# Performance work log

Measured on AMD Instinct MI355X. Metric: run time of the kernel, lower is better.

## Reference

```python
import jax, jax.numpy as jnp
import numpy as np

N = 20000   # nodes
E = 160000  # edges
D = 128     # out_dim == in_dim
H = 8       # heads
DK = D // H # 16


def setup_inputs() -> dict:
    key = jax.random.key(0)
    ks = jax.random.split(key, 16)
    f = lambda i, shape, s=1.0: jax.random.normal(ks[i], shape, dtype=jnp.float32) * s
    z = lambda shape: jnp.zeros(shape, dtype=jnp.float32)
    return {
        "x_txt": f(0, (N, D)), "x_img": f(1, (N, D)), "x_s": f(2, (N, D)),
        "Wk": f(3, (D, D), 0.05), "bk": z((D,)),
        "Wq": f(4, (D, D), 0.05), "bq": z((D,)),
        "Wv": f(5, (D, D), 0.05), "bv": z((D,)),
        "Wa": f(6, (D, D), 0.05), "ba": z((D,)),
        "rel_att": f(7, (H, DK, DK), 0.25),
        "rel_msg": f(8, (H, DK, DK), 0.25),
        "rel_pri": jnp.ones((H,), jnp.float32),
        "wm_txt": f(9, (H, DK, DK), 0.25),
        "wm_img": f(10, (H, DK, DK), 0.25),
        "wm_s": f(11, (H, DK, DK), 0.25),
        "skip": jnp.ones((1,), jnp.float32),
        "src": jax.random.randint(ks[12], (E,), 0, N),
        "dst": jax.random.randint(ks[13], (E,), 0, N),
    }


def reference(x_txt, x_img, x_s, Wk, bk, Wq, bq, Wv, bv, Wa, ba,
              rel_att, rel_msg, rel_pri, wm_txt, wm_img, wm_s, skip, src, dst):
    n_heads, dk = rel_att.shape[0], rel_att.shape[1]
    n_nodes = x_txt.shape[0]
    sqrt_dk = jnp.sqrt(jnp.asarray(dk, jnp.float32))

    def proj(x, W, b):
        return (x @ W + b).reshape(n_nodes, n_heads, dk)

    xs = (x_txt, x_img, x_s)
    k = [proj(x, Wk, bk)[src] for x in xs]  # [E,H,dk] gathered at src
    q = [proj(x, Wq, bq)[dst] for x in xs]  # [E,H,dk] gathered at dst
    v = [proj(x, Wv, bv)[src] for x in xs]

    # cross-modal lambda: per-edge modality alignment softmax (over the 3 modalities)
    wm = (wm_txt, wm_img, wm_s)
    lam_scores = jnp.stack(
        [jnp.einsum('ehd,hdf,ehf->eh', k[m], wm[m], q[m]) for m in range(3)], axis=0)
    lam = jax.nn.softmax(lam_scores, axis=0)  # [3,E,H]

    # edge attention logits (scaled *10 as in reduce_func) and relation-msg values
    att = [jnp.einsum('ehd,hdf,ehf->eh', k[m], rel_att, q[m]) * rel_pri / sqrt_dk * 10.0
           for m in range(3)]
    vmsg = [jnp.einsum('ehd,hdf->ehf', v[m], rel_msg) for m in range(3)]

    align = -(jnp.abs(att[0] - att[1]) + jnp.abs(att[0] - att[2])
              + jnp.abs(att[1] - att[2])) / 3.0

    def seg_softmax(x):  # softmax over edges sharing the same dst node
        m = jax.ops.segment_max(x, dst, num_segments=n_nodes)
        m = jnp.where(jnp.isfinite(m), m, 0.0)
        e = jnp.exp(x - m[dst])
        s = jax.ops.segment_sum(e, dst, num_segments=n_nodes)
        s = jnp.where(s == 0.0, 1.0, s)
        return e / s[dst]

    beta2 = seg_softmax(align)
    sm = [seg_softmax(a) for a in att]
    beta1 = sm[0] * lam[0] + sm[1] * lam[1] + sm[2] * lam[2]
    beta = seg_softmax(beta1 * beta2)  # [E,H]

    alpha = jax.nn.sigmoid(skip)  # [1]
    outs = []
    for m in range(3):
        h = jax.ops.segment_sum(beta[..., None] * vmsg[m], dst,
                                num_segments=n_nodes).reshape(n_nodes, -1)
        outs.append((h @ Wa + ba) * alpha + xs[m] * (1.0 - alpha))
    return tuple(outs)
```

## Files before the change

kernel.cpp:

```cpp
#include <hip/hip_runtime.h>

#define D 128
#define NH 8

typedef __bf16 bf16x8 __attribute__((ext_vector_type(8)));
typedef unsigned short ushortx8 __attribute__((ext_vector_type(8)));
typedef float floatx4 __attribute__((ext_vector_type(4)));

__device__ __forceinline__ float bf2f(unsigned short u) {
  union { unsigned int i; float f; } x; x.i = ((unsigned int)u) << 16; return x.f;
}
__device__ __forceinline__ unsigned short f2bf(float f) {
  union { float f; unsigned int i; } x; x.f = f;
  unsigned int i = x.i;
  return (unsigned short)((i + 0x7FFFu + ((i >> 16) & 1u)) >> 16);
}
__device__ __forceinline__ void acc2(unsigned int ku, unsigned int qu, float& s) {
  union { unsigned int i; float f; } a, b;
  a.i = ku << 16;          b.i = qu << 16;          s += a.f * b.f;
  a.i = ku & 0xffff0000u;  b.i = qu & 0xffff0000u;  s += a.f * b.f;
}

__global__ __launch_bounds__(256) void k_misc(
    const float* __restrict__ Wk, const float* __restrict__ bk,
    const float* __restrict__ Wq, const float* __restrict__ bq,
    const float* __restrict__ Wv, const float* __restrict__ bv,
    const float* __restrict__ rel_att, const float* __restrict__ rel_msg,
    const float* __restrict__ rel_pri,
    const float* __restrict__ wm0, const float* __restrict__ wm1,
    const float* __restrict__ wm2,
    unsigned short* __restrict__ Wt_all, float* __restrict__ bias_all,
    const int* __restrict__ dst, int* __restrict__ counts, int E)
{
  int b = blockIdx.x;
  if (b >= 384) {
    int e = (b - 384) * 256 + threadIdx.x;
    if (e < E) atomicAdd(&counts[dst[e]], 1);
    return;
  }
  int gid = b * 256 + threadIdx.x;
  if (gid >= 6 * 128 * 128) return;
  int p = gid >> 14;
  int idx = gid & 16383;
  int c = idx >> 7, k = idx & 127;
  int h = c >> 4, r = c & 15;
  float wsum = 0.f, bsum = 0.f;
  if (p == 0) {
    wsum = Wk[k * 128 + c];
    bsum = bk[c];
  } else if (p <= 4) {
    const float* M = (p == 1) ? rel_att : ((p == 2) ? wm0 : ((p == 3) ? wm1 : wm2));
#pragma unroll
    for (int f = 0; f < 16; f++) {
      float mv = M[h * 256 + r * 16 + f];
      wsum += Wq[k * 128 + h * 16 + f] * mv;
      bsum += bq[h * 16 + f] * mv;
    }
    if (p == 1) { float sc = rel_pri[h] * 2.5f; wsum *= sc; bsum *= sc; }
  } else {
#pragma unroll
    for (int d = 0; d < 16; d++) {
      float mv = rel_msg[h * 256 + d * 16 + r];
      wsum += Wv[k * 128 + h * 16 + d] * mv;
      bsum += bv[h * 16 + d] * mv;
    }
  }
  Wt_all[(size_t)p * 16384 + c * 128 + k] = f2bf(wsum);
  if (k == 0) bias_all[p * 128 + c] = bsum;
}

__global__ __launch_bounds__(256) void k_proj(
    const float* __restrict__ x0, const float* __restrict__ x1,
    const float* __restrict__ x2,
    const unsigned short* __restrict__ Wt_all, const float* __restrict__ bias_all,
    unsigned short* __restrict__ P, int N)
{
  __shared__ __attribute__((aligned(16))) unsigned short Wt[128 * 136];
  int m = blockIdx.y;
  const float* X = (m == 0) ? x0 : ((m == 1) ? x1 : x2);
  int tid = threadIdx.x;
  int wave = tid >> 6, lane = tid & 63;
  int quad = lane >> 4, l16 = lane & 15;
  int row0 = blockIdx.x * 64 + wave * 16;
  int arow = row0 + l16; if (arow >= N) arow = N - 1;
  const float* ap = X + (size_t)arow * D;
  bf16x8 afr[4];
#pragma unroll
  for (int kk4 = 0; kk4 < 4; kk4++) {
    float4 f0 = *(const float4*)(ap + kk4 * 32 + quad * 8);
    float4 f1 = *(const float4*)(ap + kk4 * 32 + quad * 8 + 4);
    ushortx8 uu;
    uu[0]=f2bf(f0.x); uu[1]=f2bf(f0.y); uu[2]=f2bf(f0.z); uu[3]=f2bf(f0.w);
    uu[4]=f2bf(f1.x); uu[5]=f2bf(f1.y); uu[6]=f2bf(f1.z); uu[7]=f2bf(f1.w);
    afr[kk4] = __builtin_bit_cast(bf16x8, uu);
  }
  for (int pt = 0; pt < 4; pt++) {
    int wp = (pt == 0) ? 0 : ((pt == 1) ? 1 : ((pt == 2) ? (2 + m) : 5));
    const unsigned short* Wsrc = Wt_all + (size_t)wp * 16384;
    const float* B = bias_all + wp * 128;
    __syncthreads();
#pragma unroll
    for (int it = 0; it < 8; it++) {
      int idx = it * 256 + tid;
      int c = idx >> 4, kc = (idx & 15) << 3;
      *(uint4*)(&Wt[c * 136 + kc]) = *(const uint4*)(&Wsrc[c * 128 + kc]);
    }
    __syncthreads();
    floatx4 acc[8];
#pragma unroll
    for (int ct = 0; ct < 8; ct++) acc[ct] = (floatx4)0.f;
#pragma unroll
    for (int kk4 = 0; kk4 < 4; kk4++) {
#pragma unroll
      for (int ct = 0; ct < 8; ct++) {
        uint4 bu = *(const uint4*)(&Wt[(ct * 16 + l16) * 136 + kk4 * 32 + quad * 8]);
        bf16x8 bf = __builtin_bit_cast(bf16x8, bu);
        acc[ct] = __builtin_amdgcn_mfma_f32_16x16x32_bf16(afr[kk4], bf, acc[ct], 0, 0, 0);
      }
    }
    unsigned short* Pout = P + (size_t)(pt * 3 + m) * N * D;
#pragma unroll
    for (int ct = 0; ct < 8; ct++) {
      int col = ct * 16 + l16;
      float bias = B[col];
#pragma unroll
      for (int i = 0; i < 4; i++) {
        int r = row0 + quad * 4 + i;
        if (r < N) Pout[(size_t)r * D + col] = f2bf(acc[ct][i] + bias);
      }
    }
  }
}

__global__ __launch_bounds__(1024) void k_scan_part(
    const int* __restrict__ counts, int* __restrict__ row_start,
    int* __restrict__ partials, int N)
{
  __shared__ int wsum[16];
  int tid = threadIdx.x;
  int gi = blockIdx.x * 1024 + tid;
  int v = (gi < N) ? counts[gi] : 0;
  int lane = tid & 63, wid = tid >> 6;
  int x = v;
#pragma unroll
  for (int off = 1; off < 64; off <<= 1) {
    int y = __shfl_up(x, off, 64);
    if (lane >= off) x += y;
  }
  if (lane == 63) wsum[wid] = x;
  __syncthreads();
  if (wid == 0) {
    int ws = (lane < 16) ? wsum[lane] : 0;
#pragma unroll
    for (int off = 1; off < 16; off <<= 1) {
      int y = __shfl_up(ws, off, 64);
      if (lane >= off) ws += y;
    }
    if (lane < 16) wsum[lane] = ws;
  }
  __syncthreads();
  int excl = x - v + (wid > 0 ? wsum[wid - 1] : 0);
  if (gi <= N) row_start[gi] = excl;
  if (tid == 0) partials[blockIdx.x] = wsum[15];
}

__global__ __launch_bounds__(1024) void k_scan_fix(
    int* __restrict__ row_start, const int* __restrict__ partials, int N, int nb)
{
  __shared__ int offs[64];
  int tid = threadIdx.x;
  if (tid == 0) {
    int acc = 0;
    for (int b = 0; b < nb; b++) { offs[b] = acc; acc += partials[b]; }
  }
  __syncthreads();
  for (int i = tid; i <= N; i += 1024) row_start[i] += offs[i >> 10];
}

__global__ void k_scatter(const int* __restrict__ dst, const int* __restrict__ src,
                          const int* __restrict__ row_start,
                          int* __restrict__ cursor, int* __restrict__ src_sorted, int E) {
  int e = blockIdx.x * 256 + threadIdx.x;
  if (e < E) {
    int d = dst[e];
    int pos = atomicAdd(&cursor[d], 1);
    src_sorted[row_start[d] + pos] = src[e];
  }
}

__device__ __forceinline__ void edge_vals(
    const unsigned short* __restrict__ P, size_t Nsz, int s, int h,
    const uint4 (&qa)[3][2], const uint4 (&qw)[3][2],
    float (&av)[3], float (&lv)[3])
{
#pragma unroll
  for (int m = 0; m < 3; m++) {
    const unsigned short* kp = P + ((size_t)m * Nsz + s) * 128 + h * 16;
    uint4 k0 = *(const uint4*)kp, k1 = *(const uint4*)(kp + 8);
    const unsigned int* ka = (const unsigned int*)&k0;
    const unsigned int* kb = (const unsigned int*)&k1;
    const unsigned int* a0 = (const unsigned int*)&qa[m][0];
    const unsigned int* a1 = (const unsigned int*)&qa[m][1];
    const unsigned int* w0 = (const unsigned int*)&qw[m][0];
    const unsigned int* w1 = (const unsigned int*)&qw[m][1];
    float da = 0.f, dw = 0.f;
#pragma unroll
    for (int j = 0; j < 4; j++) {
      acc2(ka[j], a0[j], da); acc2(kb[j], a1[j], da);
      acc2(ka[j], w0[j], dw); acc2(kb[j], w1[j], dw);
    }
    av[m] = da;
    lv[m] = dw;
  }
  float mx = fmaxf(lv[0], fmaxf(lv[1], lv[2]));
  float e0 = __expf(lv[0] - mx), e1 = __expf(lv[1] - mx), e2 = __expf(lv[2] - mx);
  float inv = 1.f / (e0 + e1 + e2);
  lv[0] = e0 * inv; lv[1] = e1 * inv; lv[2] = e2 * inv;
}

__global__ __launch_bounds__(256) void k_node(
    const unsigned short* __restrict__ P,
    const int* __restrict__ row_start, const int* __restrict__ srcs,
    unsigned short* __restrict__ hagg, int N, int E)
{
  int tid = threadIdx.x;
  int wave = tid >> 6, lane = tid & 63;
  int n = blockIdx.x * 4 + wave;
  if (n >= N) return;
  int ro = row_start[n];
  int deg = row_start[n + 1] - ro;
  float acc00 = 0, acc01 = 0, acc10 = 0, acc11 = 0, acc20 = 0, acc21 = 0;
  if (deg > 0) {
    int h = lane & 7, slot = lane >> 3;
    size_t Nsz = (size_t)N;
    uint4 qa[3][2], qw[3][2];
#pragma unroll
    for (int m = 0; m < 3; m++) {
      const unsigned short* qap = P + ((size_t)(3 + m) * Nsz + n) * 128 + h * 16;
      const unsigned short* qwp = P + ((size_t)(6 + m) * Nsz + n) * 128 + h * 16;
      qa[m][0] = *(const uint4*)qap; qa[m][1] = *(const uint4*)(qap + 8);
      qw[m][0] = *(const uint4*)qwp; qw[m][1] = *(const uint4*)(qwp + 8);
    }
    int nch = (deg + 7) >> 3;
    float cX0[4] = {}, cX1[4] = {}, cX2[4] = {}, cEa[4] = {}, cT[4] = {};
    int cS[4] = {};
    float sA0 = 0, sA1 = 0, sA2 = 0, sAl = 0;
#pragma unroll
    for (int c = 0; c < 4; c++) {
      int idx = c * 8 + slot;
      if (c < nch && idx < deg) {
        int s = srcs[ro + idx]; cS[c] = s;
        float av[3], lv[3];
        edge_vals(P, Nsz, s, h, qa, qw, av, lv);
        float e0 = __expf(av[0]), e1 = __expf(av[1]), e2 = __expf(av[2]);
        float align = -(fabsf(av[0]-av[1]) + fabsf(av[0]-av[2]) + fabsf(av[1]-av[2])) * (1.f/3.f);
        float ea = __expf(align);
        cX0[c] = lv[0] * e0; cX1[c] = lv[1] * e1; cX2[c] = lv[2] * e2; cEa[c] = ea;
        sA0 += e0; sA1 += e1; sA2 += e2; sAl += ea;
      }
    }
    for (int c = 4; c < nch; c++) {
      int idx = c * 8 + slot;
      if (idx < deg) {
        int s = srcs[ro + idx];
        float av[3], lv[3];
        edge_vals(P, Nsz, s, h, qa, qw, av, lv);
        float align = -(fabsf(av[0]-av[1]) + fabsf(av[0]-av[2]) + fabsf(av[1]-av[2])) * (1.f/3.f);
        sA0 += __expf(av[0]); sA1 += __expf(av[1]); sA2 += __expf(av[2]);
        sAl += __expf(align);
      }
    }
#pragma unroll
    for (int off = 8; off < 64; off <<= 1) {
      sA0 += __shfl_xor(sA0, off, 64);
      sA1 += __shfl_xor(sA1, off, 64);
      sA2 += __shfl_xor(sA2, off, 64);
      sAl += __shfl_xor(sAl, off, 64);
    }
    float rA0 = 1.f / fmaxf(sA0, 1e-30f), rA1 = 1.f / fmaxf(sA1, 1e-30f);
    float rA2 = 1.f / fmaxf(sA2, 1e-30f), rAl = 1.f / fmaxf(sAl, 1e-30f);
    float sT = 0;
#pragma unroll
    for (int c = 0; c < 4; c++) {
      int idx = c * 8 + slot;
      if (c < nch && idx < deg) {
        float t = (cX0[c] * rA0 + cX1[c] * rA1 + cX2[c] * rA2) * (cEa[c] * rAl);
        cT[c] = t;
        sT += __expf(t);
      }
    }
    for (int c = 4; c < nch; c++) {
      int idx = c * 8 + slot;
      if (idx < deg) {
        int s = srcs[ro + idx];
        float av[3], lv[3];
        edge_vals(P, Nsz, s, h, qa, qw, av, lv);
        float align = -(fabsf(av[0]-av[1]) + fabsf(av[0]-av[2]) + fabsf(av[1]-av[2])) * (1.f/3.f);
        float t = (lv[0]*__expf(av[0])*rA0 + lv[1]*__expf(av[1])*rA1 + lv[2]*__expf(av[2])*rA2)
                  * (__expf(align) * rAl);
        sT += __expf(t);
      }
    }
#pragma unroll
    for (int off = 8; off < 64; off <<= 1) sT += __shfl_xor(sT, off, 64);
    float rT = 1.f / fmaxf(sT, 1e-30f);
    const unsigned int* Pu = (const unsigned int*)P;
    int hl = lane >> 3;
#pragma unroll
    for (int c = 0; c < 4; c++) {
      if (c < nch) {
        int idx = c * 8 + slot;
        float beta = (idx < deg) ? __expf(cT[c]) * rT : 0.f;
        int sv = cS[c];
        float bj[8]; int sj[8];
#pragma unroll
        for (int jj = 0; jj < 8; jj++) {
          bj[jj] = __shfl(beta, jj * 8 + hl, 64);
          sj[jj] = __shfl(sv, jj * 8, 64);
        }
#pragma unroll
        for (int jj = 0; jj < 8; jj++) {
          size_t base9 = ((size_t)9 * Nsz + sj[jj]) * 64 + lane;
          unsigned int u0 = Pu[base9];
          unsigned int u1 = Pu[base9 + Nsz * 64];
          unsigned int u2 = Pu[base9 + 2 * Nsz * 64];
          float b = bj[jj];
          acc00 += b * bf2f((unsigned short)u0); acc01 += b * bf2f((unsigned short)(u0 >> 16));
          acc10 += b * bf2f((unsigned short)u1); acc11 += b * bf2f((unsigned short)(u1 >> 16));
          acc20 += b * bf2f((unsigned short)u2); acc21 += b * bf2f((unsigned short)(u2 >> 16));
        }
      }
    }
    for (int c = 4; c < nch; c++) {
      int idx = c * 8 + slot;
      float beta = 0.f; int sv = 0;
      if (idx < deg) {
        sv = srcs[ro + idx];
        float av[3], lv[3];
        edge_vals(P, Nsz, sv, h, qa, qw, av, lv);
        float align = -(fabsf(av[0]-av[1]) + fabsf(av[0]-av[2]) + fabsf(av[1]-av[2])) * (1.f/3.f);
        float t = (lv[0]*__expf(av[0])*rA0 + lv[1]*__expf(av[1])*rA1 + lv[2]*__expf(av[2])*rA2)
                  * (__expf(align) * rAl);
        beta = __expf(t) * rT;
      }
      int jmax = min(8, deg - c * 8);
      for (int jj = 0; jj < jmax; jj++) {
        float b = __shfl(beta, jj * 8 + hl, 64);
        int s = __shfl(sv, jj * 8, 64);
        size_t base9 = ((size_t)9 * Nsz + s) * 64 + lane;
        unsigned int u0 = Pu[base9];
        unsigned int u1 = Pu[base9 + Nsz * 64];
        unsigned int u2 = Pu[base9 + 2 * Nsz * 64];
        acc00 += b * bf2f((unsigned short)u0); acc01 += b * bf2f((unsigned short)(u0 >> 16));
        acc10 += b * bf2f((unsigned short)u1); acc11 += b * bf2f((unsigned short)(u1 >> 16));
        acc20 += b * bf2f((unsigned short)u2); acc21 += b * bf2f((unsigned short)(u2 >> 16));
      }
    }
  }
  unsigned int* ho = (unsigned int*)hagg;
  ho[((size_t)0 * N + n) * 64 + lane] = ((unsigned int)f2bf(acc01) << 16) | f2bf(acc00);
  ho[((size_t)1 * N + n) * 64 + lane] = ((unsigned int)f2bf(acc11) << 16) | f2bf(acc10);
  ho[((size_t)2 * N + n) * 64 + lane] = ((unsigned int)f2bf(acc21) << 16) | f2bf(acc20);
}

__global__ __launch_bounds__(256) void k_out(
    const unsigned short* __restrict__ Hagg, const float* __restrict__ Wa,
    const float* __restrict__ ba,
    const float* __restrict__ x0, const float* __restrict__ x1,
    const float* __restrict__ x2, const float* __restrict__ skip,
    float* __restrict__ out, int N)
{
  __shared__ __attribute__((aligned(16))) unsigned short Wt[128 * 136];
  int m = blockIdx.y;
  const float* X = (m == 0) ? x0 : ((m == 1) ? x1 : x2);
  int tid = threadIdx.x;
#pragma unroll
  for (int it = 0; it < 16; it++) {
    int idx = it * 256 + tid;
    int k = idx >> 5, c4 = (idx & 31) << 2;
    float4 w = *(const float4*)(&Wa[k * 128 + c4]);
    Wt[(c4 + 0) * 136 + k] = f2bf(w.x);
    Wt[(c4 + 1) * 136 + k] = f2bf(w.y);
    Wt[(c4 + 2) * 136 + k] = f2bf(w.z);
    Wt[(c4 + 3) * 136 + k] = f2bf(w.w);
  }
  __syncthreads();
  float alpha = 1.f / (1.f + __expf(-skip[0]));
  float oma = 1.f - alpha;
  int wave = tid >> 6, lane = tid & 63;
  int quad = lane >> 4, l16 = lane & 15;
  int row0 = blockIdx.x * 64 + wave * 16;
  int arow = row0 + l16; if (arow >= N) arow = N - 1;
  const unsigned short* hp = Hagg + ((size_t)m * N + arow) * D;
  floatx4 acc[8];
#pragma unroll
  for (int ct = 0; ct < 8; ct++) acc[ct] = (floatx4)0.f;
#pragma unroll
  for (int kk = 0; kk < 128; kk += 32) {
    uint4 au = *(const uint4*)(hp + kk + quad * 8);
    bf16x8 af = __builtin_bit_cast(bf16x8, au);
#pragma unroll
    for (int ct = 0; ct < 8; ct++) {
      uint4 bu = *(const uint4*)(&Wt[(ct * 16 + l16) * 136 + kk + quad * 8]);
      bf16x8 bf = __builtin_bit_cast(bf16x8, bu);
      acc[ct] = __builtin_amdgcn_mfma_f32_16x16x32_bf16(af, bf, acc[ct], 0, 0, 0);
    }
  }
  float* om = out + (size_t)m * N * D;
#pragma unroll
  for (int ct = 0; ct < 8; ct++) {
    int col = ct * 16 + l16;
    float bias = ba[col];
#pragma unroll
    for (int i = 0; i < 4; i++) {
      int r = row0 + quad * 4 + i;
      if (r < N) {
        om[(size_t)r * D + col] =
            (acc[ct][i] + bias) * alpha + X[(size_t)r * D + col] * oma;
      }
    }
  }
}

extern "C" void kernel_launch(void* const* d_in, const int* in_sizes, int n_in,
                              void* d_out, int out_size, void* d_ws, size_t ws_size,
                              hipStream_t stream) {
  const float* x0 = (const float*)d_in[0];
  const float* x1 = (const float*)d_in[1];
  const float* x2 = (const float*)d_in[2];
  const float* Wk = (const float*)d_in[3];
  const float* bk = (const float*)d_in[4];
  const float* Wq = (const float*)d_in[5];
  const float* bq = (const float*)d_in[6];
  const float* Wv = (const float*)d_in[7];
  const float* bv = (const float*)d_in[8];
  const float* Wa = (const float*)d_in[9];
  const float* ba = (const float*)d_in[10];
  const float* rel_att = (const float*)d_in[11];
  const float* rel_msg = (const float*)d_in[12];
  const float* rel_pri = (const float*)d_in[13];
  const float* wm0 = (const float*)d_in[14];
  const float* wm1 = (const float*)d_in[15];
  const float* wm2 = (const float*)d_in[16];
  const float* skip = (const float*)d_in[17];
  const int* src = (const int*)d_in[18];
  const int* dstv = (const int*)d_in[19];
  int N = in_sizes[0] / D;
  int E = in_sizes[18];

  char* wsb = (char*)d_ws;
  size_t off = 0;
  auto alloc = [&](size_t bytes) { size_t o = off; off += (bytes + 63) & ~(size_t)63; return o; };
  unsigned short* P         = (unsigned short*)(wsb + alloc((size_t)12 * N * D * 2));
  unsigned short* Wt_all    = (unsigned short*)(wsb + alloc((size_t)6 * 16384 * 2));
  float*          bias_all  = (float*)(wsb + alloc((size_t)6 * 128 * 4));
  int*            cnt2      = (int*)(wsb + alloc((size_t)2 * N * 4));
  int*            row_start = (int*)(wsb + alloc((size_t)(N + 1) * 4));
  int*            src_sorted= (int*)(wsb + alloc((size_t)E * 4));
  int*            partials  = (int*)(wsb + alloc((size_t)64 * 4));
  unsigned short* hagg      = (unsigned short*)(wsb + alloc((size_t)3 * N * D * 2));
  int* counts = cnt2;
  int* cursor = cnt2 + N;

  hipMemsetAsync(cnt2, 0, (size_t)2 * N * sizeof(int), stream);
  int hist_blocks = (E + 255) / 256;
  k_misc<<<dim3(384 + hist_blocks), 256, 0, stream>>>(
      Wk, bk, Wq, bq, Wv, bv, rel_att, rel_msg, rel_pri, wm0, wm1, wm2,
      Wt_all, bias_all, dstv, counts, E);
  k_proj<<<dim3((N + 63) / 64, 3), 256, 0, stream>>>(
      x0, x1, x2, Wt_all, bias_all, P, N);
  int nb = (N + 1024) / 1024;
  k_scan_part<<<dim3(nb), 1024, 0, stream>>>(counts, row_start, partials, N);
  k_scan_fix<<<dim3(1), 1024, 0, stream>>>(row_start, partials, N, nb);
  k_scatter<<<dim3((E + 255) / 256), 256, 0, stream>>>(dstv, src, row_start, cursor, src_sorted, E);
  k_node<<<dim3((N + 3) / 4), 256, 0, stream>>>(
      P, row_start, src_sorted, hagg, N, E);
  k_out<<<dim3((N + 63) / 64, 3), 256, 0, stream>>>(
      hagg, Wa, ba, x0, x1, x2, skip, (float*)d_out, N);
}
```

Before: 256.3 us.

## Fold CSR scan into projection kernel, stage queries in LDS, enlarge blocks

Replaces the two-kernel prefix scan with a single-block atomic-allocated per-wave scan that runs as an extra grid row inside the projection kernel. Row segments become unordered in src_sorted, so degree is read from counts instead of row_start differences. Node kernel stages per-node query vectors in LDS rather than registers, keeps two cached chunks instead of four, and sets a minimum-occupancy launch bound to cut register pressure. Projection and output GEMM kernels move to 512-thread blocks covering 128 rows. This trades launch overhead and register use for a serial single-block scan and extra LDS reads.

```diff
diff --git a/kernel.cpp b/kernel.cpp
--- a/kernel.cpp
+++ b/kernel.cpp
@@ -69,19 +69,41 @@
   if (k == 0) bias_all[p * 128 + c] = bsum;
 }
 
-__global__ __launch_bounds__(256) void k_proj(
+__global__ __launch_bounds__(512) void k_proj(
     const float* __restrict__ x0, const float* __restrict__ x1,
     const float* __restrict__ x2,
     const unsigned short* __restrict__ Wt_all, const float* __restrict__ bias_all,
-    unsigned short* __restrict__ P, int N)
+    unsigned short* __restrict__ P,
+    const int* __restrict__ counts, int* __restrict__ row_start,
+    int* __restrict__ alloc, int N)
 {
+  if (blockIdx.y == 3) {
+    if (blockIdx.x != 0) return;
+    int tid = threadIdx.x, lane = tid & 63;
+    for (int base = 0; base < N; base += 512) {
+      int n = base + tid;
+      int cnt = (n < N) ? counts[n] : 0;
+      int x = cnt;
+#pragma unroll
+      for (int off = 1; off < 64; off <<= 1) {
+        int y = __shfl_up(x, off, 64);
+        if (lane >= off) x += y;
+      }
+      int wtot = __shfl(x, 63, 64);
+      int wbase = 0;
+      if (lane == 63) wbase = atomicAdd(alloc, wtot);
+      wbase = __shfl(wbase, 63, 64);
+      if (n < N) row_start[n] = wbase + x - cnt;
+    }
+    return;
+  }
   __shared__ __attribute__((aligned(16))) unsigned short Wt[128 * 136];
   int m = blockIdx.y;
   const float* X = (m == 0) ? x0 : ((m == 1) ? x1 : x2);
   int tid = threadIdx.x;
   int wave = tid >> 6, lane = tid & 63;
   int quad = lane >> 4, l16 = lane & 15;
-  int row0 = blockIdx.x * 64 + wave * 16;
+  int row0 = blockIdx.x * 128 + wave * 16;
   int arow = row0 + l16; if (arow >= N) arow = N - 1;
   const float* ap = X + (size_t)arow * D;
   bf16x8 afr[4];
@@ -100,8 +122,8 @@
     const float* B = bias_all + wp * 128;
     __syncthreads();
 #pragma unroll
-    for (int it = 0; it < 8; it++) {
-      int idx = it * 256 + tid;
+    for (int it = 0; it < 4; it++) {
+      int idx = it * 512 + tid;
       int c = idx >> 4, kc = (idx & 15) << 3;
       *(uint4*)(&Wt[c * 136 + kc]) = *(const uint4*)(&Wsrc[c * 128 + kc]);
     }
@@ -130,51 +152,6 @@
       }
     }
   }
-}
-
-__global__ __launch_bounds__(1024) void k_scan_part(
-    const int* __restrict__ counts, int* __restrict__ row_start,
-    int* __restrict__ partials, int N)
-{
-  __shared__ int wsum[16];
-  int tid = threadIdx.x;
-  int gi = blockIdx.x * 1024 + tid;
-  int v = (gi < N) ? counts[gi] : 0;
-  int lane = tid & 63, wid = tid >> 6;
-  int x = v;
-#pragma unroll
-  for (int off = 1; off < 64; off <<= 1) {
-    int y = __shfl_up(x, off, 64);
-    if (lane >= off) x += y;
-  }
-  if (lane == 63) wsum[wid] = x;
-  __syncthreads();
-  if (wid == 0) {
-    int ws = (lane < 16) ? wsum[lane] : 0;
-#pragma unroll
-    for (int off = 1; off < 16; off <<= 1) {
-      int y = __shfl_up(ws, off, 64);
-      if (lane >= off) ws += y;
-    }
-    if (lane < 16) wsum[lane] = ws;
-  }
-  __syncthreads();
-  int excl = x - v + (wid > 0 ? wsum[wid - 1] : 0);
-  if (gi <= N) row_start[gi] = excl;
-  if (tid == 0) partials[blockIdx.x] = wsum[15];
-}
-
-__global__ __launch_bounds__(1024) void k_scan_fix(
-    int* __restrict__ row_start, const int* __restrict__ partials, int N, int nb)
-{
-  __shared__ int offs[64];
-  int tid = threadIdx.x;
-  if (tid == 0) {
-    int acc = 0;
-    for (int b = 0; b < nb; b++) { offs[b] = acc; acc += partials[b]; }
-  }
-  __syncthreads();
-  for (int i = tid; i <= N; i += 1024) row_start[i] += offs[i >> 10];
 }
 
 __global__ void k_scatter(const int* __restrict__ dst, const int* __restrict__ src,
@@ -188,26 +165,28 @@
   }
 }
 
-__device__ __forceinline__ void edge_vals(
+__device__ __forceinline__ void edge_vals_lds(
     const unsigned short* __restrict__ P, size_t Nsz, int s, int h,
-    const uint4 (&qa)[3][2], const uint4 (&qw)[3][2],
+    const uint4* __restrict__ q,
     float (&av)[3], float (&lv)[3])
 {
 #pragma unroll
   for (int m = 0; m < 3; m++) {
     const unsigned short* kp = P + ((size_t)m * Nsz + s) * 128 + h * 16;
     uint4 k0 = *(const uint4*)kp, k1 = *(const uint4*)(kp + 8);
+    uint4 a0 = q[m * 16 + h * 2], a1 = q[m * 16 + h * 2 + 1];
+    uint4 w0 = q[(3 + m) * 16 + h * 2], w1 = q[(3 + m) * 16 + h * 2 + 1];
     const unsigned int* ka = (const unsigned int*)&k0;
     const unsigned int* kb = (const unsigned int*)&k1;
-    const unsigned int* a0 = (const unsigned int*)&qa[m][0];
-    const unsigned int* a1 = (const unsigned int*)&qa[m][1];
-    const unsigned int* w0 = (const unsigned int*)&qw[m][0];
-    const unsigned int* w1 = (const unsigned int*)&qw[m][1];
+    const unsigned int* pa0 = (const unsigned int*)&a0;
+    const unsigned int* pa1 = (const unsigned int*)&a1;
+    const unsigned int* pw0 = (const unsigned int*)&w0;
+    const unsigned int* pw1 = (const unsigned int*)&w1;
     float da = 0.f, dw = 0.f;
 #pragma unroll
     for (int j = 0; j < 4; j++) {
-      acc2(ka[j], a0[j], da); acc2(kb[j], a1[j], da);
-      acc2(ka[j], w0[j], dw); acc2(kb[j], w1[j], dw);
+      acc2(ka[j], pa0[j], da); acc2(kb[j], pa1[j], da);
+      acc2(ka[j], pw0[j], dw); acc2(kb[j], pw1[j], dw);
     }
     av[m] = da;
     lv[m] = dw;
@@ -218,40 +197,39 @@
   lv[0] = e0 * inv; lv[1] = e1 * inv; lv[2] = e2 * inv;
 }
 
-__global__ __launch_bounds__(256) void k_node(
+__global__ __launch_bounds__(256, 5) void k_node(
     const unsigned short* __restrict__ P,
-    const int* __restrict__ row_start, const int* __restrict__ srcs,
+    const int* __restrict__ row_start, const int* __restrict__ counts,
+    const int* __restrict__ srcs,
     unsigned short* __restrict__ hagg, int N, int E)
 {
+  __shared__ __attribute__((aligned(16))) uint4 qsh[4 * 96];
   int tid = threadIdx.x;
   int wave = tid >> 6, lane = tid & 63;
   int n = blockIdx.x * 4 + wave;
   if (n >= N) return;
   int ro = row_start[n];
-  int deg = row_start[n + 1] - ro;
+  int deg = counts[n];
   float acc00 = 0, acc01 = 0, acc10 = 0, acc11 = 0, acc20 = 0, acc21 = 0;
   if (deg > 0) {
     int h = lane & 7, slot = lane >> 3;
     size_t Nsz = (size_t)N;
-    uint4 qa[3][2], qw[3][2];
-#pragma unroll
-    for (int m = 0; m < 3; m++) {
-      const unsigned short* qap = P + ((size_t)(3 + m) * Nsz + n) * 128 + h * 16;
-      const unsigned short* qwp = P + ((size_t)(6 + m) * Nsz + n) * 128 + h * 16;
-      qa[m][0] = *(const uint4*)qap; qa[m][1] = *(const uint4*)(qap + 8);
-      qw[m][0] = *(const uint4*)qwp; qw[m][1] = *(const uint4*)(qwp + 8);
+    uint4* q = &qsh[wave * 96];
+    for (int idx = lane; idx < 96; idx += 64) {
+      int row = idx >> 4, col = idx & 15;
+      q[idx] = *(const uint4*)(P + ((size_t)(3 + row) * Nsz + n) * 128 + col * 8);
     }
     int nch = (deg + 7) >> 3;
-    float cX0[4] = {}, cX1[4] = {}, cX2[4] = {}, cEa[4] = {}, cT[4] = {};
-    int cS[4] = {};
+    float cX0[2] = {}, cX1[2] = {}, cX2[2] = {}, cEa[2] = {}, cT[2] = {};
+    int cS[2] = {};
     float sA0 = 0, sA1 = 0, sA2 = 0, sAl = 0;
 #pragma unroll
-    for (int c = 0; c < 4; c++) {
+    for (int c = 0; c < 2; c++) {
       int idx = c * 8 + slot;
       if (c < nch && idx < deg) {
         int s = srcs[ro + idx]; cS[c] = s;
         float av[3], lv[3];
-        edge_vals(P, Nsz, s, h, qa, qw, av, lv);
+        edge_vals_lds(P, Nsz, s, h, q, av, lv);
         float e0 = __expf(av[0]), e1 = __expf(av[1]), e2 = __expf(av[2]);
         float align = -(fabsf(av[0]-av[1]) + fabsf(av[0]-av[2]) + fabsf(av[1]-av[2])) * (1.f/3.f);
         float ea = __expf(align);
@@ -259,12 +237,12 @@
         sA0 += e0; sA1 += e1; sA2 += e2; sAl += ea;
       }
     }
-    for (int c = 4; c < nch; c++) {
+    for (int c = 2; c < nch; c++) {
       int idx = c * 8 + slot;
       if (idx < deg) {
         int s = srcs[ro + idx];
         float av[3], lv[3];
-        edge_vals(P, Nsz, s, h, qa, qw, av, lv);
+        edge_vals_lds(P, Nsz, s, h, q, av, lv);
         float align = -(fabsf(av[0]-av[1]) + fabsf(av[0]-av[2]) + fabsf(av[1]-av[2])) * (1.f/3.f);
         sA0 += __expf(av[0]); sA1 += __expf(av[1]); sA2 += __expf(av[2]);
         sAl += __expf(align);
@@ -281,7 +259,7 @@
     float rA2 = 1.f / fmaxf(sA2, 1e-30f), rAl = 1.f / fmaxf(sAl, 1e-30f);
     float sT = 0;
 #pragma unroll
-    for (int c = 0; c < 4; c++) {
+    for (int c = 0; c < 2; c++) {
       int idx = c * 8 + slot;
       if (c < nch && idx < deg) {
         float t = (cX0[c] * rA0 + cX1[c] * rA1 + cX2[c] * rA2) * (cEa[c] * rAl);
@@ -289,12 +267,12 @@
         sT += __expf(t);
       }
     }
-    for (int c = 4; c < nch; c++) {
+    for (int c = 2; c < nch; c++) {
       int idx = c * 8 + slot;
       if (idx < deg) {
         int s = srcs[ro + idx];
         float av[3], lv[3];
-        edge_vals(P, Nsz, s, h, qa, qw, av, lv);
+        edge_vals_lds(P, Nsz, s, h, q, av, lv);
         float align = -(fabsf(av[0]-av[1]) + fabsf(av[0]-av[2]) + fabsf(av[1]-av[2])) * (1.f/3.f);
         float t = (lv[0]*__expf(av[0])*rA0 + lv[1]*__expf(av[1])*rA1 + lv[2]*__expf(av[2])*rA2)
                   * (__expf(align) * rAl);
@@ -307,7 +285,7 @@
     const unsigned int* Pu = (const unsigned int*)P;
     int hl = lane >> 3;
 #pragma unroll
-    for (int c = 0; c < 4; c++) {
+    for (int c = 0; c < 2; c++) {
       if (c < nch) {
         int idx = c * 8 + slot;
         float beta = (idx < deg) ? __expf(cT[c]) * rT : 0.f;
@@ -331,13 +309,13 @@
         }
       }
     }
-    for (int c = 4; c < nch; c++) {
+    for (int c = 2; c < nch; c++) {
       int idx = c * 8 + slot;
       float beta = 0.f; int sv = 0;
       if (idx < deg) {
         sv = srcs[ro + idx];
         float av[3], lv[3];
-        edge_vals(P, Nsz, sv, h, qa, qw, av, lv);
+        edge_vals_lds(P, Nsz, sv, h, q, av, lv);
         float align = -(fabsf(av[0]-av[1]) + fabsf(av[0]-av[2]) + fabsf(av[1]-av[2])) * (1.f/3.f);
         float t = (lv[0]*__expf(av[0])*rA0 + lv[1]*__expf(av[1])*rA1 + lv[2]*__expf(av[2])*rA2)
                   * (__expf(align) * rAl);
@@ -363,7 +341,7 @@
   ho[((size_t)2 * N + n) * 64 + lane] = ((unsigned int)f2bf(acc21) << 16) | f2bf(acc20);
 }
 
-__global__ __launch_bounds__(256) void k_out(
+__global__ __launch_bounds__(512) void k_out(
     const unsigned short* __restrict__ Hagg, const float* __restrict__ Wa,
     const float* __restrict__ ba,
     const float* __restrict__ x0, const float* __restrict__ x1,
@@ -375,8 +353,8 @@
   const float* X = (m == 0) ? x0 : ((m == 1) ? x1 : x2);
   int tid = threadIdx.x;
 #pragma unroll
-  for (int it = 0; it < 16; it++) {
-    int idx = it * 256 + tid;
+  for (int it = 0; it < 8; it++) {
+    int idx = it * 512 + tid;
     int k = idx >> 5, c4 = (idx & 31) << 2;
     float4 w = *(const float4*)(&Wa[k * 128 + c4]);
     Wt[(c4 + 0) * 136 + k] = f2bf(w.x);
@@ -389,7 +367,7 @@
   float oma = 1.f - alpha;
   int wave = tid >> 6, lane = tid & 63;
   int quad = lane >> 4, l16 = lane & 15;
-  int row0 = blockIdx.x * 64 + wave * 16;
+  int row0 = blockIdx.x * 128 + wave * 16;
   int arow = row0 + l16; if (arow >= N) arow = N - 1;
   const unsigned short* hp = Hagg + ((size_t)m * N + arow) * D;
   floatx4 acc[8];
@@ -450,31 +428,29 @@
 
   char* wsb = (char*)d_ws;
   size_t off = 0;
-  auto alloc = [&](size_t bytes) { size_t o = off; off += (bytes + 63) & ~(size_t)63; return o; };
-  unsigned short* P         = (unsigned short*)(wsb + alloc((size_t)12 * N * D * 2));
-  unsigned short* Wt_all    = (unsigned short*)(wsb + alloc((size_t)6 * 16384 * 2));
-  float*          bias_all  = (float*)(wsb + alloc((size_t)6 * 128 * 4));
-  int*            cnt2      = (int*)(wsb + alloc((size_t)2 * N * 4));
-  int*            row_start = (int*)(wsb + alloc((size_t)(N + 1) * 4));
-  int*            src_sorted= (int*)(wsb + alloc((size_t)E * 4));
-  int*            partials  = (int*)(wsb + alloc((size_t)64 * 4));
-  unsigned short* hagg      = (unsigned short*)(wsb + alloc((size_t)3 * N * D * 2));
+  auto alloc_b = [&](size_t bytes) { size_t o = off; off += (bytes + 63) & ~(size_t)63; return o; };
+  unsigned short* P         = (unsigned short*)(wsb + alloc_b((size_t)12 * N * D * 2));
+  unsigned short* Wt_all    = (unsigned short*)(wsb + alloc_b((size_t)6 * 16384 * 2));
+  float*          bias_all  = (float*)(wsb + alloc_b((size_t)6 * 128 * 4));
+  int*            cnt2      = (int*)(wsb + alloc_b(((size_t)2 * N + 64) * 4));
+  int*            row_start = (int*)(wsb + alloc_b((size_t)(N + 1) * 4));
+  int*            src_sorted= (int*)(wsb + alloc_b((size_t)E * 4));
+  unsigned short* hagg      = (unsigned short*)(wsb + alloc_b((size_t)3 * N * D * 2));
   int* counts = cnt2;
   int* cursor = cnt2 + N;
-
-  hipMemsetAsync(cnt2, 0, (size_t)2 * N * sizeof(int), stream);
+  int* allocc = cnt2 + 2 * N;
+
+  hipMemsetAsync(cnt2, 0, ((size_t)2 * N + 64) * sizeof(int), stream);
   int hist_blocks = (E + 255) / 256;
   k_misc<<<dim3(384 + hist_blocks), 256, 0, stream>>>(
       Wk, bk, Wq, bq, Wv, bv, rel_att, rel_msg, rel_pri, wm0, wm1, wm2,
       Wt_all, bias_all, dstv, counts, E);
-  k_proj<<<dim3((N + 63) / 64, 3), 256, 0, stream>>>(
-      x0, x1, x2, Wt_all, bias_all, P, N);
-  int nb = (N + 1024) / 1024;
-  k_scan_part<<<dim3(nb), 1024, 0, stream>>>(counts, row_start, partials, N);
-  k_scan_fix<<<dim3(1), 1024, 0, stream>>>(row_start, partials, N, nb);
-  k_scatter<<<dim3((E + 255) / 256), 256, 0, stream>>>(dstv, src, row_start, cursor, src_sorted, E);
+  k_proj<<<dim3((N + 127) / 128, 4), 512, 0, stream>>>(
+      x0, x1, x2, Wt_all, bias_all, P, counts, row_start, allocc, N);
+  k_scatter<<<dim3((E + 255) / 256), 256, 0, stream>>>(
+      dstv, src, row_start, cursor, src_sorted, E);
   k_node<<<dim3((N + 3) / 4), 256, 0, stream>>>(
-      P, row_start, src_sorted, hagg, N, E);
-  k_out<<<dim3((N + 63) / 64, 3), 256, 0, stream>>>(
+      P, row_start, counts, src_sorted, hagg, N, E);
+  k_out<<<dim3((N + 127) / 128, 3), 512, 0, stream>>>(
       hagg, Wa, ba, x0, x1, x2, skip, (float*)d_out, N);
 }
```

After: 265.1 us. +3.5%, slower.
